# Kernel optimization log

Hardware: AMD Instinct MI355X
Metric: run time of the kernel (lower is better)

## Reference

```python
import jax, jax.numpy as jnp
import numpy as np

# Model hyperparameters (match init_kwargs)
T = 3          # reasoning hops
L = 3          # rule channels (parallel LSTMs)
E = 50000      # number of entities
N = 1000000    # number of KG triples
R = 200        # r_size = (n-1)//2
NREL = 2 * R + 1  # n = 401 (forward rels, inverse rels, identity)
H = 256        # emb_size
TAU = 10.0     # tau_1 softmax temperature
TOPK = 1000    # top-k state pruning for hops t>=1
B = 8          # batch size


def setup_inputs() -> dict:
    key = jax.random.key(0)
    ks = jax.random.split(key, 16)
    s = 0.05
    return {
        "input_x": jax.random.randint(ks[0], (B,), 0, E),
        "input_r": jax.random.randint(ks[1], (B,), 0, NREL),
        "e2triple": jax.random.randint(ks[2], (3, N), 0, E),
        "triple2e": jax.random.randint(ks[3], (2, N), 0, E),
        "r2triple": jax.random.randint(ks[4], (1, N), 0, R),
        "emb": jax.random.normal(ks[5], (NREL, H), jnp.float32) * s,
        "Wih_f": jax.random.normal(ks[6], (L, 4 * H, H), jnp.float32) * s,
        "Whh_f": jax.random.normal(ks[7], (L, 4 * H, H), jnp.float32) * s,
        "bih_f": jax.random.normal(ks[8], (L, 4 * H), jnp.float32) * s,
        "bhh_f": jax.random.normal(ks[9], (L, 4 * H), jnp.float32) * s,
        "Wih_b": jax.random.normal(ks[10], (L, 4 * H, H), jnp.float32) * s,
        "Whh_b": jax.random.normal(ks[11], (L, 4 * H, H), jnp.float32) * s,
        "bih_b": jax.random.normal(ks[12], (L, 4 * H), jnp.float32) * s,
        "bhh_b": jax.random.normal(ks[13], (L, 4 * H), jnp.float32) * s,
        "linW": jax.random.normal(ks[14], (NREL, 2 * H), jnp.float32) * s,
        "linb": jax.random.normal(ks[15], (NREL,), jnp.float32) * s,
    }


def _lstm_scan(x, Wih, Whh, bih, bhh):
    # x: [S, B, H]; PyTorch gate order i, f, g, o. Returns hidden seq [S, B, H].
    Bn = x.shape[1]
    Hh = Whh.shape[1]
    pre = x @ Wih.T + bih + bhh  # hoist input projection out of the scan

    def step(carry, xt):
        h, c = carry
        g = xt + h @ Whh.T
        i, f, gg, o = jnp.split(g, 4, axis=-1)
        c = jax.nn.sigmoid(f) * c + jax.nn.sigmoid(i) * jnp.tanh(gg)
        h = jax.nn.sigmoid(o) * jnp.tanh(c)
        return (h, c), h

    init = (jnp.zeros((Bn, Hh), x.dtype), jnp.zeros((Bn, Hh), x.dtype))
    _, hs = jax.lax.scan(step, init, pre)
    return hs


def reference(input_x, input_r, e2triple, triple2e, r2triple, emb,
              Wih_f, Whh_f, bih_f, bhh_f, Wih_b, Whh_b, bih_b, bhh_b,
              linW, linb):
    Bsz = input_x.shape[0]
    x0 = jax.nn.one_hot(input_x, E, dtype=emb.dtype)  # [B, E] one-hot query entity
    q = emb[input_r]                                   # [B, H] query relation emb
    # [T+1, B, H]: T copies of the query rel emb, last step is the special emb[-1]
    seq = jnp.concatenate([
        jnp.broadcast_to(q[None], (T, Bsz, H)),
        jnp.broadcast_to(emb[-1][None, None, :], (1, Bsz, H)),
    ], axis=0)

    outs = []
    for l in range(L):  # small fixed number of structurally distinct LSTMs
        hf = _lstm_scan(seq, Wih_f[l], Whh_f[l], bih_f[l], bhh_f[l])
        hb = _lstm_scan(seq[::-1], Wih_b[l], Whh_b[l], bih_b[l], bhh_b[l])[::-1]
        rnn = jnp.concatenate([hf, hb], axis=-1).transpose(1, 0, 2)  # [B, T+1, 2H]
        outs.append(rnn[:, :-1] @ linW.T + linb)                      # [B, T, n]
    w_all = jnp.stack(outs, axis=2)  # [B, T, L, n]

    heads = e2triple[0]   # [N] head entity per triple
    tails = triple2e[1]   # [N] tail entity per triple
    tails2 = e2triple[2]  # [N] tail entity per triple (inverse-direction gather)
    rels = r2triple[0]    # [N] relation per triple, in [0, R)

    def propagate(x, w):
        # x: [B, *, E] entity state, w: [B, L, n] relation weights
        s_i = w[:, :, -1:] * x                              # identity relation
        msg_f = x[:, :, heads] * w[:, :, rels]              # [B, L, N] fwd messages
        s_h = jnp.zeros((Bsz, L, E), x.dtype).at[:, :, tails].add(msg_f)
        msg_b = x[:, :, tails2] * w[:, :, rels + R]         # inverse relations
        s_t = jnp.zeros((Bsz, L, E), x.dtype).at[:, :, heads].add(msg_b)
        return s_i + s_h + s_t

    def prune_topk(x, k):
        # keep top-k entity scores per (batch, channel), zero the rest
        th = jax.lax.top_k(x, k)[0][..., -1:]
        return jnp.where(x >= th, x, jnp.zeros((), x.dtype))

    s = None
    for t in range(T):
        w = jax.nn.softmax(w_all[:, t] / TAU, axis=-1)      # [B, L, n]
        xin = x0[:, None, :] if t == 0 else prune_topk(s, TOPK)
        st = propagate(xin, w)
        s = st / jnp.maximum(st.sum(-1, keepdims=True), 1e-7)
    return s.sum(axis=1)  # [B, E]
```

## Files before the change

kernel.cpp:

```cpp
#include <hip/hip_runtime.h>
#include <math.h>

#define TT 3
#define LL 3
#define EE 50000
#define NN 1000000
#define RR 200
#define NRELC 401
#define HH 256
#define BB 8
#define KTOP 1000
#define SROW 24
#define NBUCK 782
#define BSH 6
#define CSRN (2 * NN)
#define STB 512
#define SEGS 50176

__device__ __forceinline__ float sigmoidf_(float x) {
    if (x >= 0.f) { return 1.f / (1.f + expf(-x)); }
    float z = expf(x); return z / (1.f + z);
}

__global__ __launch_bounds__(256) void pre_fused(
    const int* __restrict__ input_r, const float* __restrict__ emb,
    const float* __restrict__ Wih_f, const float* __restrict__ bih_f, const float* __restrict__ bhh_f,
    const float* __restrict__ Wih_b, const float* __restrict__ bih_b, const float* __restrict__ bhh_b,
    float* __restrict__ preq, float* __restrict__ pree,
    float* __restrict__ hstate, float* __restrict__ cstate, float* __restrict__ hbuf2,
    const int* __restrict__ heads, const int* __restrict__ tails,
    unsigned* __restrict__ bh, int do_hist)
{
    if (blockIdx.x >= 384) {
        if (!do_hist) return;
        __shared__ unsigned h[NBUCK];
        int tid = threadIdx.x;
        int bid = blockIdx.x - 384;
        for (int i = tid; i < NBUCK; i += 256) h[i] = 0u;
        __syncthreads();
        for (int i = bid * 256 + tid; i < NN; i += STB * 256) {
            atomicAdd(&h[tails[i] >> BSH], 1u);
            atomicAdd(&h[heads[i] >> BSH], 1u);
        }
        __syncthreads();
        for (int j = tid; j < NBUCK; j += 256)
            bh[(size_t)j * STB + bid] = h[j];
        return;
    }
    int wave = blockIdx.x * 4 + (threadIdx.x >> 6);
    int lane = threadIdx.x & 63;
    int ld = wave >> 8;
    int j  = wave & 255;
    int l = ld >> 1, dir = ld & 1;
    const float* Wih = (dir ? Wih_b : Wih_f) + (size_t)l * 4 * HH * HH;
    const float* bih = (dir ? bih_b : bih_f) + l * 4 * HH;
    const float* bhh = (dir ? bhh_b : bhh_f) + l * 4 * HH;

    float4 xf[9];
    for (int b = 0; b < 8; ++b) {
        int r = input_r[b];
        xf[b] = *(const float4*)(emb + (size_t)r * HH + lane * 4);
    }
    xf[8] = *(const float4*)(emb + (size_t)(NRELC - 1) * HH + lane * 4);

    float g4[4], ge4[4];
    for (int q = 0; q < 4; ++q) {
        int row = q * 256 + j;
        float4 w4 = *(const float4*)(Wih + (size_t)row * HH + lane * 4);
        float acc[9];
        #pragma unroll
        for (int c = 0; c < 9; ++c)
            acc[c] = w4.x * xf[c].x + w4.y * xf[c].y + w4.z * xf[c].z + w4.w * xf[c].w;
        #pragma unroll
        for (int off = 32; off > 0; off >>= 1)
            #pragma unroll
            for (int c = 0; c < 9; ++c) acc[c] += __shfl_xor(acc[c], off);
        float bsum = bih[row] + bhh[row];
        g4[q]  = (lane < 8 ? acc[lane] : 0.f) + bsum;
        ge4[q] = acc[8] + bsum;
        if (lane < 8) preq[((size_t)ld * 8 + lane) * 1024 + row] = g4[q];
        if (lane == 8) pree[(size_t)ld * 1024 + row] = ge4[q];
    }
    if (lane < 8) {
        float gi, gg, go;
        if (dir == 0) { gi = g4[0]; gg = g4[2]; go = g4[3]; }
        else          { gi = ge4[0]; gg = ge4[2]; go = ge4[3]; }
        float c = sigmoidf_(gi) * tanhf(gg);
        float h = sigmoidf_(go) * tanhf(c);
        int g = (ld * 8 + lane) * 256 + j;
        cstate[g] = c;
        hstate[g] = h;
        if (dir == 0) hbuf2[(((size_t)ld * 8 + lane) * 3 + 0) * HH + j] = h;
    }
}

__global__ __launch_bounds__(256) void rec_fused(
    const float* __restrict__ Whh_f, const float* __restrict__ Whh_b,
    const float* __restrict__ preq, const float* __restrict__ pree,
    const float* __restrict__ hprev, float* __restrict__ hnext,
    float* __restrict__ cstate, float* __restrict__ hbuf2, int step)
{
    int wave = blockIdx.x * 4 + (threadIdx.x >> 6);
    int lane = threadIdx.x & 63;
    int ld = wave >> 8, j = wave & 255;
    int l = ld >> 1, dir = ld & 1;
    const float* Whh = (dir ? Whh_b : Whh_f) + (size_t)l * 4 * HH * HH;
    bool use_e = (dir == 0) && (step == 3);

    float4 hf[8];
    for (int b = 0; b < 8; ++b)
        hf[b] = *(const float4*)(hprev + ((size_t)ld * 8 + b) * HH + lane * 4);

    float g4[4];
    for (int q = 0; q < 4; ++q) {
        int row = q * 256 + j;
        float4 w4 = *(const float4*)(Whh + (size_t)row * HH + lane * 4);
        float acc[8];
        #pragma unroll
        for (int b = 0; b < 8; ++b)
            acc[b] = w4.x * hf[b].x + w4.y * hf[b].y + w4.z * hf[b].z + w4.w * hf[b].w;
        #pragma unroll
        for (int off = 32; off > 0; off >>= 1)
            #pragma unroll
            for (int b = 0; b < 8; ++b) acc[b] += __shfl_xor(acc[b], off);
        if (lane < 8) {
            float pre = use_e ? pree[(size_t)ld * 1024 + row]
                              : preq[((size_t)ld * 8 + lane) * 1024 + row];
            g4[q] = acc[lane] + pre;
        }
    }
    if (lane < 8) {
        int g = (ld * 8 + lane) * 256 + j;
        float c = cstate[g];
        float iv = sigmoidf_(g4[0]), fv = sigmoidf_(g4[1]);
        float gg = tanhf(g4[2]),     ov = sigmoidf_(g4[3]);
        c = fv * c + iv * gg;
        float h = ov * tanhf(c);
        cstate[g] = c;
        hnext[g] = h;
        int t_out = dir ? (3 - step) : step;
        if (t_out <= 2) hbuf2[(((size_t)ld * 8 + lane) * 3 + t_out) * HH + j] = h;
    }
}

__global__ __launch_bounds__(256) void logits_dot(
    const float* __restrict__ hbuf2, const float* __restrict__ linW,
    const float* __restrict__ linb, float* __restrict__ wbuf)
{
    int wave = blockIdx.x * 4 + (threadIdx.x >> 6);
    if (wave >= 3 * 3 * NRELC) return;
    int lane = threadIdx.x & 63;
    int n = wave % NRELC;
    int tc = wave / NRELC;
    int t = tc / 3, chunk = tc % 3;
    const float4* wr = (const float4*)(linW + (size_t)n * 2 * HH + lane * 8);
    float4 w4a = wr[0], w4b = wr[1];
    float acc[8];
    #pragma unroll
    for (int i = 0; i < 8; ++i) {
        int combo = chunk * 8 + i;
        int b = combo / 3, l = combo % 3;
        int ldh = (lane < 32) ? (l * 2 + 0) : (l * 2 + 1);
        const float* hsrc = hbuf2 + (((size_t)ldh * 8 + b) * 3 + t) * HH + (lane & 31) * 8;
        float4 f0 = *(const float4*)hsrc;
        float4 f1 = *(const float4*)(hsrc + 4);
        acc[i] = w4a.x * f0.x + w4a.y * f0.y + w4a.z * f0.z + w4a.w * f0.w
               + w4b.x * f1.x + w4b.y * f1.y + w4b.z * f1.z + w4b.w * f1.w;
    }
    #pragma unroll
    for (int off = 32; off > 0; off >>= 1)
        #pragma unroll
        for (int i = 0; i < 8; ++i) acc[i] += __shfl_xor(acc[i], off);
    if (lane < 8) {
        int combo = chunk * 8 + lane;
        wbuf[((size_t)t * 24 + combo) * NRELC + n] = acc[lane] + linb[n];
    }
}

__global__ __launch_bounds__(256) void softmax_kernel(
    float* __restrict__ wbuf, float* __restrict__ wT0,
    int* __restrict__ maskT0, int* __restrict__ maskT1, int* __restrict__ maskT2,
    const int* __restrict__ input_x, unsigned* __restrict__ rowcnt)
{
    int tid = threadIdx.x;
    if (blockIdx.x >= 72) {
        if (maskT0 == nullptr) return;
        __shared__ int xs[8];
        if (tid < 8) xs[tid] = input_x[tid];
        if (blockIdx.x == 72 && tid < 24) rowcnt[tid] = 0u;
        __syncthreads();
        int e = (blockIdx.x - 72) * 256 + tid;
        if (e >= EE) return;
        int m = 0;
        #pragma unroll
        for (int b = 0; b < 8; ++b) if (e == xs[b]) m |= 1 << b;
        maskT0[e] = m;
        maskT1[e] = 0;
        maskT2[e] = 0;
        return;
    }
    int rowi = blockIdx.x;
    float* w = wbuf + (size_t)rowi * NRELC;
    __shared__ float red[256];
    float v0 = w[tid];
    float v1 = (tid + 256 < NRELC) ? w[tid + 256] : -1e30f;
    red[tid] = fmaxf(v0, v1); __syncthreads();
    for (int s2 = 128; s2 > 0; s2 >>= 1) {
        if (tid < s2) red[tid] = fmaxf(red[tid], red[tid + s2]);
        __syncthreads();
    }
    float m = red[0]; __syncthreads();
    float e0 = expf((v0 - m) * 0.1f);
    float e1 = (tid + 256 < NRELC) ? expf((v1 - m) * 0.1f) : 0.f;
    red[tid] = e0 + e1; __syncthreads();
    for (int s2 = 128; s2 > 0; s2 >>= 1) {
        if (tid < s2) red[tid] += red[tid + s2];
        __syncthreads();
    }
    float denom = red[0];
    float o0 = e0 / denom;
    w[tid] = o0;
    float o1 = 0.f;
    if (tid + 256 < NRELC) { o1 = e1 / denom; w[tid + 256] = o1; }
    if (wT0 != nullptr && rowi < 24) {
        if (tid < 2 * RR) wT0[(size_t)tid * SROW + rowi] = o0;
        if (tid + 256 < 2 * RR) wT0[(size_t)(tid + 256) * SROW + rowi] = o1;
    }
}

__global__ __launch_bounds__(256) void fill_seed(
    float* __restrict__ s, const int* __restrict__ input_x, const float* __restrict__ w0,
    unsigned* __restrict__ rowcnt)
{
    __shared__ int xs[8];
    __shared__ float wv[24];
    if (threadIdx.x < 8) xs[threadIdx.x] = input_x[threadIdx.x];
    if (threadIdx.x < 24) wv[threadIdx.x] = w0[(size_t)threadIdx.x * NRELC + (NRELC - 1)];
    if (blockIdx.x == 0 && threadIdx.x < 24) rowcnt[threadIdx.x] = 0u;
    __syncthreads();
    int i = blockIdx.x * 256 + threadIdx.x;
    if (i >= SROW * EE) return;
    int row = i % 24;
    int e = i / 24;
    s[i] = (e == xs[row / 3]) ? wv[row] : 0.f;
}

__global__ __launch_bounds__(256) void hop0_scan(
    const int* __restrict__ heads, const int* __restrict__ tails,
    const int* __restrict__ tails2, const int* __restrict__ rels,
    const int* __restrict__ input_x, const float* __restrict__ w0,
    float* __restrict__ s)
{
    __shared__ int xs[BB];
    if (threadIdx.x < BB) xs[threadIdx.x] = input_x[threadIdx.x];
    __syncthreads();
    int i = blockIdx.x * 256 + threadIdx.x;
    if (i >= NN) return;
    int h = heads[i], t2 = tails2[i];
    bool any = false;
    #pragma unroll
    for (int b = 0; b < BB; ++b) any = any || (h == xs[b]) || (t2 == xs[b]);
    if (!any) return;
    int tl = tails[i], rr = rels[i];
    for (int b = 0; b < BB; ++b) {
        if (h == xs[b])
            for (int l = 0; l < LL; ++l)
                atomicAdd(&s[(size_t)tl * SROW + b * 3 + l], w0[(b * 3 + l) * NRELC + rr]);
        if (t2 == xs[b])
            for (int l = 0; l < LL; ++l)
                atomicAdd(&s[(size_t)h * SROW + b * 3 + l], w0[(b * 3 + l) * NRELC + rr + RR]);
    }
}

__global__ __launch_bounds__(256) void rowsum_compact(
    const float* __restrict__ s, float* __restrict__ partial,
    unsigned* __restrict__ ckey, unsigned* __restrict__ rowcnt, int do_compact)
{
    __shared__ float acc[24];
    __shared__ unsigned lkey[24][168];
    __shared__ unsigned lcnt[24];
    __shared__ unsigned lbase[24];
    int tid = threadIdx.x;
    if (tid < 24) { acc[tid] = 0.f; lcnt[tid] = 0u; }
    __syncthreads();
    int gidx = blockIdx.x * 256 + tid;
    int row = gidx % 24;
    float a = 0.f;
    const int total = SROW * EE;
    for (int k = 0; k < 13; ++k) {
        long i = (long)gidx + (long)k * 98304;
        if (i < total) {
            float v = s[i];
            a += v;
            if (do_compact && __float_as_uint(v) != 0u) {
                unsigned slot = atomicAdd(&lcnt[row], 1u);
                slot = min(slot, 167u);
                lkey[row][slot] = __float_as_uint(v);
            }
        }
    }
    if (do_compact) {
        __syncthreads();
        if (tid < 24) {
            unsigned c = min(lcnt[tid], 168u);
            lcnt[tid] = c;
            lbase[tid] = min(atomicAdd(&rowcnt[tid], c), (unsigned)SEGS);
        }
        __syncthreads();
        int r = tid % 24;
        int nthr = (r < 16) ? 11 : 10;
        unsigned cnt = lcnt[r], base = lbase[r];
        if (base + cnt > (unsigned)SEGS) cnt = (unsigned)SEGS - base;
        for (unsigned j = (unsigned)(tid / 24); j < cnt; j += nthr)
            ckey[(size_t)r * SEGS + base + j] = lkey[r][j];
        __syncthreads();
    }
    atomicAdd(&acc[row], a);
    __syncthreads();
    if (tid < 24) partial[blockIdx.x * 24 + tid] = acc[tid];
}

__global__ __launch_bounds__(256) void rowsum_fin(
    const float* __restrict__ partial, float* __restrict__ sums,
    const float* __restrict__ w_t, float* __restrict__ wsc,
    float* __restrict__ wTg)
{
    int r = blockIdx.x;
    int tid = threadIdx.x;
    __shared__ float sa;
    if (tid == 0) {
        float a = 0.f;
        for (int j = 0; j < 384; ++j) a += partial[j * 24 + r];
        a = fmaxf(a, 1e-7f);
        sums[r] = a;
        sa = a;
    }
    __syncthreads();
    if (w_t != nullptr) {
        float a = sa;
        for (int i = tid; i < NRELC; i += 256) {
            float v = w_t[(size_t)r * NRELC + i] / a;
            wsc[(size_t)r * NRELC + i] = v;
            if (wTg != nullptr && i < 2 * RR) wTg[(size_t)i * SROW + r] = v;
        }
    }
}

__global__ __launch_bounds__(256) void rowsum_fin2(
    const float* __restrict__ partial2, float* __restrict__ sums,
    const float* __restrict__ w_t, float* __restrict__ wsc,
    float* __restrict__ wTg)
{
    int r = blockIdx.x;
    int tid = threadIdx.x;
    __shared__ float red[256];
    float a = 0.f;
    for (int g = tid; g < NBUCK; g += 256) a += partial2[(size_t)g * 24 + r];
    red[tid] = a; __syncthreads();
    for (int s2 = 128; s2 > 0; s2 >>= 1) {
        if (tid < s2) red[tid] += red[tid + s2];
        __syncthreads();
    }
    __shared__ float sa;
    if (tid == 0) { sa = fmaxf(red[0], 1e-7f); sums[r] = sa; }
    __syncthreads();
    if (w_t != nullptr) {
        float aa = sa;
        for (int i = tid; i < NRELC; i += 256) {
            float v = w_t[(size_t)r * NRELC + i] / aa;
            wsc[(size_t)r * NRELC + i] = v;
            if (wTg != nullptr && i < 2 * RR) wTg[(size_t)i * SROW + r] = v;
        }
    }
}

__global__ __launch_bounds__(512) void hop_epi(
    const unsigned* __restrict__ ckey, const unsigned* __restrict__ cent,
    unsigned* __restrict__ rowcnt, float* __restrict__ th,
    int* __restrict__ mask_next,
    const float* __restrict__ partial2, float* __restrict__ sums,
    const float* __restrict__ w_t, float* __restrict__ wsc,
    float* __restrict__ wTg)
{
    int tid = threadIdx.x;
    if (blockIdx.x >= 24) {
        int r = blockIdx.x - 24;
        __shared__ float red[256];
        __shared__ float sa;
        if (tid < 256) {
            float a = 0.f;
            for (int g = tid; g < NBUCK; g += 256) a += partial2[(size_t)g * 24 + r];
            red[tid] = a;
        }
        __syncthreads();
        for (int s2 = 128; s2 > 0; s2 >>= 1) {
            if (tid < s2) red[tid] += red[tid + s2];
            __syncthreads();
        }
        if (tid == 0) { sa = fmaxf(red[0], 1e-7f); sums[r] = sa; }
        __syncthreads();
        float aa = sa;
        for (int i = tid; i < NRELC; i += 512) {
            float v = w_t[(size_t)r * NRELC + i] / aa;
            wsc[(size_t)r * NRELC + i] = v;
            if (i < 2 * RR) wTg[(size_t)i * SROW + r] = v;
        }
        return;
    }
    int row = blockIdx.x;
    const unsigned* keys = ckey + (size_t)row * SEGS;
    int n = min((int)rowcnt[row], SEGS);
    __shared__ unsigned hist[256];
    __shared__ int red[256];
    __shared__ int sh_bin, sh_rem;
    unsigned prefix = 0;
    int remk = KTOP;
    int iters = (n + 511) / 512;
    int lane = tid & 63;
    for (int round = 0; round < 4; ++round) {
        if (tid < 256) hist[tid] = 0u;
        __syncthreads();
        int shift = 24 - 8 * round;
        for (int it = 0; it < iters; ++it) {
            int i = it * 512 + tid;
            bool valid = (i < n);
            unsigned key = valid ? keys[i] : 0u;
            valid = valid && (round == 0 || (key >> (shift + 8)) == prefix);
            unsigned bin = valid ? ((key >> shift) & 255u) : 0u;
            unsigned long long peers = __ballot(valid);
            #pragma unroll
            for (int bit = 0; bit < 8; ++bit) {
                unsigned long long bm = __ballot(valid && ((bin >> bit) & 1u));
                peers &= ((bin >> bit) & 1u) ? bm : ~bm;
            }
            if (valid) {
                unsigned long long lower = peers & ((1ull << lane) - 1ull);
                if (lower == 0ull)
                    atomicAdd(&hist[bin], (unsigned)__popcll(peers));
            }
        }
        __syncthreads();
        if (tid < 256) red[tid] = (int)hist[tid];
        __syncthreads();
        for (int off = 1; off < 256; off <<= 1) {
            int v = 0;
            if (tid < 256 && tid + off < 256) v = red[tid + off];
            __syncthreads();
            if (tid < 256) red[tid] += v;
            __syncthreads();
        }
        if (tid == 0) { sh_bin = 0; sh_rem = remk; }
        __syncthreads();
        if (tid < 256) {
            int cnt = (int)hist[tid];
            int above = (tid == 255) ? 0 : red[tid + 1];
            if (above < remk && above + cnt >= remk) { sh_bin = tid; sh_rem = remk - above; }
        }
        __syncthreads();
        prefix = (prefix << 8) | (unsigned)sh_bin;
        remk = sh_rem;
        __syncthreads();
    }
    if (tid == 0) th[row] = __uint_as_float(prefix);
    {
        const unsigned* ents = cent + (size_t)row * SEGS;
        int bit = 1 << (row / 3);
        for (int i = tid; i < n; i += 512) {
            if (keys[i] >= prefix) {
                unsigned e = ents[i];
                if (e < (unsigned)EE) atomicOr(&mask_next[e], bit);
            }
        }
        if (tid == 0) rowcnt[row] = 0u;
    }
}

__global__ __launch_bounds__(512) void topk_select(
    const unsigned* __restrict__ ckey, unsigned* __restrict__ rowcnt,
    float* __restrict__ th, int* __restrict__ mask)
{
    int row = blockIdx.x, tid = threadIdx.x;
    {
        int per = (EE + 23) / 24;
        int e0 = row * per, e1 = min(e0 + per, EE);
        for (int e = e0 + tid; e < e1; e += 512) mask[e] = 0;
    }
    const unsigned* keys = ckey + (size_t)row * SEGS;
    int n = min((int)rowcnt[row], SEGS);
    __shared__ unsigned hist[256];
    __shared__ int red[256];
    __shared__ int sh_bin, sh_rem;
    unsigned prefix = 0;
    int remk = KTOP;
    int iters = (n + 511) / 512;
    int lane = tid & 63;
    for (int round = 0; round < 4; ++round) {
        if (tid < 256) hist[tid] = 0u;
        __syncthreads();
        int shift = 24 - 8 * round;
        for (int it = 0; it < iters; ++it) {
            int i = it * 512 + tid;
            bool valid = (i < n);
            unsigned key = valid ? keys[i] : 0u;
            valid = valid && (round == 0 || (key >> (shift + 8)) == prefix);
            unsigned bin = valid ? ((key >> shift) & 255u) : 0u;
            unsigned long long peers = __ballot(valid);
            #pragma unroll
            for (int bit = 0; bit < 8; ++bit) {
                unsigned long long bm = __ballot(valid && ((bin >> bit) & 1u));
                peers &= ((bin >> bit) & 1u) ? bm : ~bm;
            }
            if (valid) {
                unsigned long long lower = peers & ((1ull << lane) - 1ull);
                if (lower == 0ull)
                    atomicAdd(&hist[bin], (unsigned)__popcll(peers));
            }
        }
        __syncthreads();
        if (tid < 256) red[tid] = (int)hist[tid];
        __syncthreads();
        for (int off = 1; off < 256; off <<= 1) {
            int v = 0;
            if (tid < 256 && tid + off < 256) v = red[tid + off];
            __syncthreads();
            if (tid < 256) red[tid] += v;
            __syncthreads();
        }
        if (tid == 0) { sh_bin = 0; sh_rem = remk; }
        __syncthreads();
        if (tid < 256) {
            int cnt = (int)hist[tid];
            int above = (tid == 255) ? 0 : red[tid + 1];
            if (above < remk && above + cnt >= remk) { sh_bin = tid; sh_rem = remk - above; }
        }
        __syncthreads();
        prefix = (prefix << 8) | (unsigned)sh_bin;
        remk = sh_rem;
        __syncthreads();
    }
    if (tid == 0) th[row] = __uint_as_float(prefix);
}

__global__ __launch_bounds__(256) void prune_flat(
    float* __restrict__ s, const float* __restrict__ th,
    const float* __restrict__ wsc, float* __restrict__ x, int* __restrict__ mask,
    unsigned* __restrict__ rowcnt, int write_s)
{
    __shared__ float ths[24], w4s[24];
    if (threadIdx.x < 24) {
        ths[threadIdx.x] = th[threadIdx.x];
        w4s[threadIdx.x] = wsc[threadIdx.x * NRELC + (NRELC - 1)];
    }
    if (blockIdx.x == 0 && threadIdx.x < 24) rowcnt[threadIdx.x] = 0u;
    __syncthreads();
    int i = blockIdx.x * 256 + threadIdx.x;
    if (i >= SROW * EE) return;
    int row = i % 24;
    int e = i / 24;
    float v = s[i];
    float xv = (v >= ths[row]) ? v : 0.f;
    x[i] = xv;
    if (write_s) s[i] = w4s[row] * xv;
    if (xv > 0.f) atomicOr(&mask[e], 1 << (row / 3));
}

__global__ __launch_bounds__(256) void hop_scan(
    const int* __restrict__ heads, const int* __restrict__ tails,
    const int* __restrict__ tails2, const int* __restrict__ rels,
    const int* __restrict__ mask, const float* __restrict__ x,
    const float* __restrict__ wsc, float* __restrict__ s)
{
    int gid = blockIdx.x * 256 + threadIdx.x;
    int i = gid >> 3;
    if (i >= NN) return;
    int b = gid & 7;
    int h = heads[i], t2 = tails2[i];
    int mh = mask[h], mt = mask[t2];
    bool ah = (mh >> b) & 1;
    bool at = (mt >> b) & 1;
    if (!(ah || at)) return;
    int tl = tails[i], rr = rels[i];
    int row = b * 3;
    if (ah) {
        float v0 = x[(size_t)h * SROW + row];
        float v1 = x[(size_t)h * SROW + row + 1];
        float v2 = x[(size_t)h * SROW + row + 2];
        if (v0 != 0.f) atomicAdd(&s[(size_t)tl * SROW + row],     v0 * wsc[(row)     * NRELC + rr]);
        if (v1 != 0.f) atomicAdd(&s[(size_t)tl * SROW + row + 1], v1 * wsc[(row + 1) * NRELC + rr]);
        if (v2 != 0.f) atomicAdd(&s[(size_t)tl * SROW + row + 2], v2 * wsc[(row + 2) * NRELC + rr]);
    }
    if (at) {
        float v0 = x[(size_t)t2 * SROW + row];
        float v1 = x[(size_t)t2 * SROW + row + 1];
        float v2 = x[(size_t)t2 * SROW + row + 2];
        if (v0 != 0.f) atomicAdd(&s[(size_t)h * SROW + row],     v0 * wsc[(row)     * NRELC + rr + RR]);
        if (v1 != 0.f) atomicAdd(&s[(size_t)h * SROW + row + 1], v1 * wsc[(row + 1) * NRELC + rr + RR]);
        if (v2 != 0.f) atomicAdd(&s[(size_t)h * SROW + row + 2], v2 * wsc[(row + 2) * NRELC + rr + RR]);
    }
}

__global__ __launch_bounds__(512) void csr_scanb(
    unsigned* __restrict__ bh, unsigned* __restrict__ gcnt)
{
    __shared__ unsigned sc[STB];
    int bk = blockIdx.x, tid = threadIdx.x;
    unsigned v = bh[(size_t)bk * STB + tid];
    sc[tid] = v; __syncthreads();
    #pragma unroll
    for (int o = 1; o < STB; o <<= 1) {
        unsigned u = (tid >= o) ? sc[tid - o] : 0u;
        __syncthreads();
        sc[tid] += u;
        __syncthreads();
    }
    bh[(size_t)bk * STB + tid] = sc[tid] - v;
    if (tid == STB - 1) gcnt[bk] = sc[tid];
}

__global__ __launch_bounds__(1024) void csr_scan2(
    const unsigned* __restrict__ gcnt, unsigned* __restrict__ gOff)
{
    __shared__ unsigned sc[1024];
    int tid = threadIdx.x;
    unsigned v = (tid < NBUCK) ? gcnt[tid] : 0u;
    sc[tid] = v; __syncthreads();
    #pragma unroll
    for (int o = 1; o < 1024; o <<= 1) {
        unsigned u = (tid >= o) ? sc[tid - o] : 0u;
        __syncthreads();
        sc[tid] += u;
        __syncthreads();
    }
    if (tid < NBUCK) gOff[tid] = sc[tid] - v;
    if (tid == NBUCK - 1) gOff[NBUCK] = sc[tid];
}

__global__ __launch_bounds__(256) void csr_stage2(
    const int* __restrict__ heads, const int* __restrict__ tails,
    const int* __restrict__ tails2, const int* __restrict__ rels,
    const unsigned* __restrict__ gOff, const unsigned* __restrict__ bh,
    unsigned* __restrict__ staging)
{
    __shared__ unsigned base[NBUCK];
    __shared__ unsigned cur[NBUCK];
    int tid = threadIdx.x;
    for (int j = tid; j < NBUCK; j += 256) {
        base[j] = gOff[j] + bh[(size_t)j * STB + blockIdx.x];
        cur[j] = 0u;
    }
    __syncthreads();
    for (int i = blockIdx.x * 256 + tid; i < NN; i += STB * 256) {
        unsigned rl = (unsigned)rels[i];
        int h = heads[i], d1 = tails[i], t2 = tails2[i];
        unsigned p1 = base[d1 >> BSH] + atomicAdd(&cur[d1 >> BSH], 1u);
        if (p1 < (unsigned)CSRN)
            staging[p1] = ((unsigned)(d1 & 63) << 26) | ((unsigned)h << 9) | rl;
        unsigned p2 = base[h >> BSH] + atomicAdd(&cur[h >> BSH], 1u);
        if (p2 < (unsigned)CSRN)
            staging[p2] = ((unsigned)(h & 63) << 26) | ((unsigned)t2 << 9) | (rl + RR);
    }
}

__global__ __launch_bounds__(256) void hop_bucket(
    const unsigned* __restrict__ gOff, const unsigned* __restrict__ staging,
    const int* __restrict__ mask, const float* __restrict__ sprev,
    const float* __restrict__ th, const int* __restrict__ input_x,
    const float* __restrict__ wT, const float* __restrict__ wsc,
    float* __restrict__ snext, float* __restrict__ partial2,
    unsigned* __restrict__ ckey, unsigned* __restrict__ cent,
    unsigned* __restrict__ rowcnt, int do_compact, int is_t0)
{
    __shared__ float sl[64][24];
    __shared__ float w4s[24];
    __shared__ float ths[24];
    __shared__ int   xs8[8];
    __shared__ float acc24[24];
    __shared__ unsigned lcnt[24];
    __shared__ unsigned lbase[24];
    __shared__ unsigned lkey[24][64];
    __shared__ unsigned lent[24][64];
    int bk = blockIdx.x, tid = threadIdx.x;
    for (int i = tid; i < 64 * 24; i += 256) ((float*)sl)[i] = 0.f;
    if (tid < 24) {
        w4s[tid] = wsc[tid * NRELC + (NRELC - 1)];
        ths[tid] = is_t0 ? 0.f : th[tid];
        acc24[tid] = 0.f;
        lcnt[tid] = 0u;
    }
    if (tid < 8) xs8[tid] = is_t0 ? input_x[tid] : 0;
    __syncthreads();
    unsigned j0 = gOff[bk], j1 = gOff[bk + 1];
    for (unsigned j = j0 + tid; j < j1; j += 256) {
        unsigned p = staging[j];
        int src = (int)((p >> 9) & 0xFFFFu);
        int m = mask[src];
        if (!m) continue;
        int dl = (int)(p >> 26);
        int rel = (int)(p & 511u);
        const float* wr = wT + (size_t)rel * SROW;
        if (is_t0) {
            while (m) {
                int b = __ffs(m) - 1; m &= m - 1;
                int r = b * 3;
                atomicAdd(&sl[dl][r],     wr[r]);
                atomicAdd(&sl[dl][r + 1], wr[r + 1]);
                atomicAdd(&sl[dl][r + 2], wr[r + 2]);
            }
        } else {
            const float* xsrow = sprev + (size_t)src * SROW;
            while (m) {
                int b = __ffs(m) - 1; m &= m - 1;
                int r = b * 3;
                float x0 = xsrow[r];     x0 = (x0 >= ths[r])     ? x0 : 0.f;
                float x1 = xsrow[r + 1]; x1 = (x1 >= ths[r + 1]) ? x1 : 0.f;
                float x2 = xsrow[r + 2]; x2 = (x2 >= ths[r + 2]) ? x2 : 0.f;
                atomicAdd(&sl[dl][r],     x0 * wr[r]);
                atomicAdd(&sl[dl][r + 1], x1 * wr[r + 1]);
                atomicAdd(&sl[dl][r + 2], x2 * wr[r + 2]);
            }
        }
    }
    __syncthreads();
    int e0 = bk * 64;
    for (int idx = tid; idx < 64 * 24; idx += 256) {
        int el = idx / 24, row = idx % 24;
        int e = e0 + el;
        if (e >= EE) continue;
        float xv;
        if (is_t0) {
            xv = (e == xs8[row / 3]) ? 1.f : 0.f;
        } else {
            float u = sprev[(size_t)e * SROW + row];
            xv = (u >= ths[row]) ? u : 0.f;
        }
        float v = sl[el][row] + w4s[row] * xv;
        snext[(size_t)e * SROW + row] = v;
        atomicAdd(&acc24[row], v);
        if (do_compact && __float_as_uint(v) != 0u) {
            unsigned slot = atomicAdd(&lcnt[row], 1u);
            slot = min(slot, 63u);
            lkey[row][slot] = __float_as_uint(v);
            lent[row][slot] = (unsigned)e;
        }
    }
    __syncthreads();
    if (tid < 24) partial2[(size_t)bk * 24 + tid] = acc24[tid];
    if (do_compact) {
        if (tid < 24) {
            unsigned c = min(lcnt[tid], 64u);
            lcnt[tid] = c;
            lbase[tid] = min(atomicAdd(&rowcnt[tid], c), (unsigned)SEGS);
        }
        __syncthreads();
        int r = tid % 24;
        int nthr = (r < 16) ? 11 : 10;
        unsigned cnt = lcnt[r], base = lbase[r];
        if (base + cnt > (unsigned)SEGS) cnt = (unsigned)SEGS - base;
        for (unsigned j = (unsigned)(tid / 24); j < cnt; j += nthr) {
            ckey[(size_t)r * SEGS + base + j] = lkey[r][j];
            cent[(size_t)r * SEGS + base + j] = lent[r][j];
        }
    }
}

__global__ void final_kernel(const float* __restrict__ s, const float* __restrict__ sums,
                             float* __restrict__ out) {
    __shared__ float ss[24];
    if (threadIdx.x < 24) ss[threadIdx.x] = sums[threadIdx.x];
    __syncthreads();
    int e = blockIdx.x * 256 + threadIdx.x;
    if (e >= EE) return;
    const float* se = s + (size_t)e * SROW;
    #pragma unroll
    for (int b = 0; b < 8; ++b)
        out[(size_t)b * EE + e] = se[b * 3] / ss[b * 3]
                                + se[b * 3 + 1] / ss[b * 3 + 1]
                                + se[b * 3 + 2] / ss[b * 3 + 2];
}

extern "C" void kernel_launch(void* const* d_in, const int* in_sizes, int n_in,
                              void* d_out, int out_size, void* d_ws, size_t ws_size,
                              hipStream_t stream)
{
    const int*   input_x  = (const int*)d_in[0];
    const int*   input_r  = (const int*)d_in[1];
    const int*   e2triple = (const int*)d_in[2];
    const int*   triple2e = (const int*)d_in[3];
    const int*   r2triple = (const int*)d_in[4];
    const float* emb      = (const float*)d_in[5];
    const float* Wih_f    = (const float*)d_in[6];
    const float* Whh_f    = (const float*)d_in[7];
    const float* bih_f    = (const float*)d_in[8];
    const float* bhh_f    = (const float*)d_in[9];
    const float* Wih_b    = (const float*)d_in[10];
    const float* Whh_b    = (const float*)d_in[11];
    const float* bih_b    = (const float*)d_in[12];
    const float* bhh_b    = (const float*)d_in[13];
    const float* linW     = (const float*)d_in[14];
    const float* linb     = (const float*)d_in[15];

    const int* heads  = e2triple;
    const int* tails2 = e2triple + 2 * (size_t)NN;
    const int* tails  = triple2e + (size_t)NN;
    const int* rels   = r2triple;

    float* ws      = (float*)d_ws;
    float* hbuf    = ws;
    float* wbuf    = hbuf + 36864;
    float* sstA    = wbuf + 28872;
    float* sstB    = sstA + 1200000;
    float* sums    = sstB + 1200000;
    float* th      = sums + 24;
    int*   maskT0  = (int*)(th + 24);
    int*   maskT1  = maskT0 + EE;
    int*   maskT2  = maskT1 + EE;
    float* partial = (float*)(maskT2 + EE);
    unsigned* rowcnt  = (unsigned*)(partial + 9216);
    float* partial2   = (float*)(rowcnt + 32);
    unsigned* ckey    = (unsigned*)(partial2 + NBUCK * 24);
    unsigned* cent    = ckey + 24 * (size_t)SEGS;
    unsigned* bh      = cent + 24 * (size_t)SEGS;
    unsigned* gcnt    = bh + (size_t)NBUCK * STB;
    unsigned* gOff    = gcnt + 784;
    unsigned* staging = gOff + 800;
    float*    wT      = (float*)(staging + CSRN);
    float*    wT0     = wT + 9600;
    const size_t NEED = (size_t)((wT0 + 9600) - ws) * 4;
    const bool use_csr = (ws_size >= NEED);
    float* wsc     = hbuf;
    float* preq    = sstA;
    float* pree    = preq + 49152;
    float* hstateA = pree + 6144;
    float* hstateB = hstateA + 12288;
    float* cstate  = hstateB + 12288;

    float* out = (float*)d_out;
    const int EBLK  = (EE + 255) / 256;
    const int SBLK  = (SROW * EE + 255) / 256;
    const int NBLK  = (NN + 255) / 256;
    const int N8BLK = (NN * 8) / 256;

    pre_fused<<<896, 256, 0, stream>>>(input_r, emb, Wih_f, bih_f, bhh_f,
                                       Wih_b, bih_b, bhh_b, preq, pree,
                                       hstateA, cstate, hbuf,
                                       heads, tails, bh, use_csr ? 1 : 0);
    rec_fused<<<384, 256, 0, stream>>>(Whh_f, Whh_b, preq, pree, hstateA, hstateB,
                                       cstate, hbuf, 1);
    rec_fused<<<384, 256, 0, stream>>>(Whh_f, Whh_b, preq, pree, hstateB, hstateA,
                                       cstate, hbuf, 2);
    rec_fused<<<384, 256, 0, stream>>>(Whh_f, Whh_b, preq, pree, hstateA, hstateB,
                                       cstate, hbuf, 3);
    logits_dot<<<903, 256, 0, stream>>>(hbuf, linW, linb, wbuf);

    if (use_csr) {
        softmax_kernel<<<72 + EBLK, 256, 0, stream>>>(wbuf, wT0, maskT0, maskT1, maskT2,
                                                      input_x, rowcnt);
        csr_scanb<<<NBUCK, 512, 0, stream>>>(bh, gcnt);
        csr_scan2<<<1, 1024, 0, stream>>>(gcnt, gOff);
        csr_stage2<<<STB, 256, 0, stream>>>(heads, tails, tails2, rels, gOff, bh, staging);
        hop_bucket<<<NBUCK, 256, 0, stream>>>(gOff, staging, maskT0, nullptr, nullptr,
                                              input_x, wT0, wbuf, sstA, partial2,
                                              ckey, cent, rowcnt, 1, 1);
        hop_epi<<<48, 512, 0, stream>>>(ckey, cent, rowcnt, th, maskT1,
                                        partial2, sums, wbuf + 1 * 24 * NRELC, wsc, wT);
        hop_bucket<<<NBUCK, 256, 0, stream>>>(gOff, staging, maskT1, sstA, th,
                                              input_x, wT, wsc, sstB, partial2,
                                              ckey, cent, rowcnt, 1, 0);
        hop_epi<<<48, 512, 0, stream>>>(ckey, cent, rowcnt, th, maskT2,
                                        partial2, sums, wbuf + 2 * 24 * NRELC, wsc, wT);
        hop_bucket<<<NBUCK, 256, 0, stream>>>(gOff, staging, maskT2, sstB, th,
                                              input_x, wT, wsc, sstA, partial2,
                                              ckey, cent, rowcnt, 0, 0);
        rowsum_fin2<<<24, 256, 0, stream>>>(partial2, sums, nullptr, nullptr, nullptr);
        final_kernel<<<EBLK, 256, 0, stream>>>(sstA, sums, out);
    } else {
        softmax_kernel<<<72, 256, 0, stream>>>(wbuf, nullptr, nullptr, nullptr, nullptr,
                                               input_x, rowcnt);
        float* xst = sstA;
        float* sst = sstB;
        int* mask = maskT0;
        fill_seed<<<SBLK, 256, 0, stream>>>(sst, input_x, wbuf, rowcnt);
        hop0_scan<<<NBLK, 256, 0, stream>>>(heads, tails, tails2, rels, input_x, wbuf, sst);
        rowsum_compact<<<384, 256, 0, stream>>>(sst, partial, ckey, rowcnt, 1);
        rowsum_fin<<<24, 256, 0, stream>>>(partial, sums, wbuf + 1 * 24 * NRELC, wsc, nullptr);
        for (int t = 1; t < TT; ++t) {
            topk_select<<<24, 512, 0, stream>>>(ckey, rowcnt, th, mask);
            prune_flat<<<SBLK, 256, 0, stream>>>(sst, th, wsc, xst, mask, rowcnt, 1);
            hop_scan<<<N8BLK, 256, 0, stream>>>(heads, tails, tails2, rels, mask, xst, wsc, sst);
            rowsum_compact<<<384, 256, 0, stream>>>(sst, partial, ckey, rowcnt,
                                                    (t + 1 < TT) ? 1 : 0);
            const float* w_next = (t + 1 < TT) ? (wbuf + (size_t)(t + 1) * 24 * NRELC) : nullptr;
            rowsum_fin<<<24, 256, 0, stream>>>(partial, sums, w_next, wsc, nullptr);
        }
        final_kernel<<<EBLK, 256, 0, stream>>>(sst, sums, out);
    }
}
```

Before: 289.4 us.

## Fuse CSR build stages into logits and softmax kernels, merge final rowsum

```diff
diff --git a/kernel.cpp b/kernel.cpp
--- a/kernel.cpp
+++ b/kernel.cpp
@@ -16,6 +16,7 @@
 #define CSRN (2 * NN)
 #define STB 512
 #define SEGS 50176
+#define EBLK ((EE + 255) / 256)
 
 __device__ __forceinline__ float sigmoidf_(float x) {
     if (x >= 0.f) { return 1.f / (1.f + expf(-x)); }
@@ -145,11 +146,35 @@
 
 __global__ __launch_bounds__(256) void logits_dot(
     const float* __restrict__ hbuf2, const float* __restrict__ linW,
-    const float* __restrict__ linb, float* __restrict__ wbuf)
-{
-    int wave = blockIdx.x * 4 + (threadIdx.x >> 6);
+    const float* __restrict__ linb, float* __restrict__ wbuf,
+    unsigned* __restrict__ bh, unsigned* __restrict__ gcnt)
+{
+    int tid = threadIdx.x;
+    if (blockIdx.x >= 903) {
+        if (gcnt == nullptr) return;
+        int bk = blockIdx.x - 903;
+        unsigned a = bh[(size_t)bk * STB + 2 * tid];
+        unsigned b = bh[(size_t)bk * STB + 2 * tid + 1];
+        unsigned s = a + b;
+        __shared__ unsigned sc[256];
+        sc[tid] = s; __syncthreads();
+        #pragma unroll
+        for (int off = 1; off < 256; off <<= 1) {
+            unsigned u = (tid >= off) ? sc[tid - off] : 0u;
+            __syncthreads();
+            sc[tid] += u;
+            __syncthreads();
+        }
+        unsigned incl = sc[tid];
+        unsigned ex = incl - s;
+        bh[(size_t)bk * STB + 2 * tid]     = ex;
+        bh[(size_t)bk * STB + 2 * tid + 1] = ex + a;
+        if (tid == 255) gcnt[bk] = incl;
+        return;
+    }
+    int wave = blockIdx.x * 4 + (tid >> 6);
     if (wave >= 3 * 3 * NRELC) return;
-    int lane = threadIdx.x & 63;
+    int lane = tid & 63;
     int n = wave % NRELC;
     int tc = wave / NRELC;
     int t = tc / 3, chunk = tc % 3;
@@ -180,9 +205,62 @@
 __global__ __launch_bounds__(256) void softmax_kernel(
     float* __restrict__ wbuf, float* __restrict__ wT0,
     int* __restrict__ maskT0, int* __restrict__ maskT1, int* __restrict__ maskT2,
-    const int* __restrict__ input_x, unsigned* __restrict__ rowcnt)
+    const int* __restrict__ input_x, unsigned* __restrict__ rowcnt,
+    const int* __restrict__ heads, const int* __restrict__ tails,
+    const int* __restrict__ tails2, const int* __restrict__ rels,
+    const unsigned* __restrict__ bh, const unsigned* __restrict__ gcnt,
+    unsigned* __restrict__ gOff, unsigned* __restrict__ staging)
 {
     int tid = threadIdx.x;
+    if (blockIdx.x >= 72 + EBLK) {
+        int bid = blockIdx.x - (72 + EBLK);
+        __shared__ unsigned sv[1024];
+        __shared__ unsigned base[NBUCK];
+        __shared__ unsigned cur[NBUCK];
+        unsigned orig[4];
+        #pragma unroll
+        for (int k = 0; k < 4; ++k) {
+            int j = tid + k * 256;
+            unsigned v = (j < NBUCK) ? gcnt[j] : 0u;
+            orig[k] = v; sv[j] = v;
+        }
+        __syncthreads();
+        for (int off = 1; off < 1024; off <<= 1) {
+            unsigned t4[4];
+            #pragma unroll
+            for (int k = 0; k < 4; ++k) {
+                int j = tid + k * 256;
+                t4[k] = (j >= off) ? sv[j - off] : 0u;
+            }
+            __syncthreads();
+            #pragma unroll
+            for (int k = 0; k < 4; ++k) sv[tid + k * 256] += t4[k];
+            __syncthreads();
+        }
+        #pragma unroll
+        for (int k = 0; k < 4; ++k) {
+            int j = tid + k * 256;
+            if (j < NBUCK) {
+                unsigned ex = sv[j] - orig[k];
+                base[j] = ex + bh[(size_t)j * STB + bid];
+                cur[j] = 0u;
+                if (bid == 0) gOff[j] = ex;
+            }
+        }
+        if (bid == 0 && tid == 0) gOff[NBUCK] = sv[1023];
+        __syncthreads();
+        for (int i = bid * 256 + tid; i < NN; i += STB * 256) {
+            unsigned rl = (unsigned)rels[i];
+            int h = heads[i], d1 = tails[i], t2 = tails2[i];
+            unsigned p1 = base[d1 >> BSH] + atomicAdd(&cur[d1 >> BSH], 1u);
+            if (p1 < (unsigned)CSRN)
+                staging[p1] = ((unsigned)(d1 & 63) << 26) | ((unsigned)h << 9) | rl;
+            unsigned p2 = base[h >> BSH] + atomicAdd(&cur[h >> BSH], 1u);
+            if (p2 < (unsigned)CSRN)
+                staging[p2] = ((unsigned)(h & 63) << 26) | ((unsigned)t2 << 9) | (rl + RR);
+        }
+        return;
+    }
     if (blockIdx.x >= 72) {
         if (maskT0 == nullptr) return;
         __shared__ int xs[8];
@@ -340,34 +418,6 @@
         float a = sa;
         for (int i = tid; i < NRELC; i += 256) {
             float v = w_t[(size_t)r * NRELC + i] / a;
-            wsc[(size_t)r * NRELC + i] = v;
-            if (wTg != nullptr && i < 2 * RR) wTg[(size_t)i * SROW + r] = v;
-        }
-    }
-}
-
-__global__ __launch_bounds__(256) void rowsum_fin2(
-    const float* __restrict__ partial2, float* __restrict__ sums,
-    const float* __restrict__ w_t, float* __restrict__ wsc,
-    float* __restrict__ wTg)
-{
-    int r = blockIdx.x;
-    int tid = threadIdx.x;
-    __shared__ float red[256];
-    float a = 0.f;
-    for (int g = tid; g < NBUCK; g += 256) a += partial2[(size_t)g * 24 + r];
-    red[tid] = a; __syncthreads();
-    for (int s2 = 128; s2 > 0; s2 >>= 1) {
-        if (tid < s2) red[tid] += red[tid + s2];
-        __syncthreads();
-    }
-    __shared__ float sa;
-    if (tid == 0) { sa = fmaxf(red[0], 1e-7f); sums[r] = sa; }
-    __syncthreads();
-    if (w_t != nullptr) {
-        float aa = sa;
-        for (int i = tid; i < NRELC; i += 256) {
-            float v = w_t[(size_t)r * NRELC + i] / aa;
             wsc[(size_t)r * NRELC + i] = v;
             if (wTg != nullptr && i < 2 * RR) wTg[(size_t)i * SROW + r] = v;
         }
@@ -596,68 +646,6 @@
         if (v0 != 0.f) atomicAdd(&s[(size_t)h * SROW + row],     v0 * wsc[(row)     * NRELC + rr + RR]);
         if (v1 != 0.f) atomicAdd(&s[(size_t)h * SROW + row + 1], v1 * wsc[(row + 1) * NRELC + rr + RR]);
         if (v2 != 0.f) atomicAdd(&s[(size_t)h * SROW + row + 2], v2 * wsc[(row + 2) * NRELC + rr + RR]);
-    }
-}
-
-__global__ __launch_bounds__(512) void csr_scanb(
-    unsigned* __restrict__ bh, unsigned* __restrict__ gcnt)
-{
-    __shared__ unsigned sc[STB];
-    int bk = blockIdx.x, tid = threadIdx.x;
-    unsigned v = bh[(size_t)bk * STB + tid];
-    sc[tid] = v; __syncthreads();
-    #pragma unroll
-    for (int o = 1; o < STB; o <<= 1) {
-        unsigned u = (tid >= o) ? sc[tid - o] : 0u;
-        __syncthreads();
-        sc[tid] += u;
-        __syncthreads();
-    }
-    bh[(size_t)bk * STB + tid] = sc[tid] - v;
-    if (tid == STB - 1) gcnt[bk] = sc[tid];
-}
-
-__global__ __launch_bounds__(1024) void csr_scan2(
-    const unsigned* __restrict__ gcnt, unsigned* __restrict__ gOff)
-{
-    __shared__ unsigned sc[1024];
-    int tid = threadIdx.x;
-    unsigned v = (tid < NBUCK) ? gcnt[tid] : 0u;
-    sc[tid] = v; __syncthreads();
-    #pragma unroll
-    for (int o = 1; o < 1024; o <<= 1) {
-        unsigned u = (tid >= o) ? sc[tid - o] : 0u;
-        __syncthreads();
-        sc[tid] += u;
-        __syncthreads();
-    }
-    if (tid < NBUCK) gOff[tid] = sc[tid] - v;
-    if (tid == NBUCK - 1) gOff[NBUCK] = sc[tid];
-}
-
-__global__ __launch_bounds__(256) void csr_stage2(
-    const int* __restrict__ heads, const int* __restrict__ tails,
-    const int* __restrict__ tails2, const int* __restrict__ rels,
-    const unsigned* __restrict__ gOff, const unsigned* __restrict__ bh,
-    unsigned* __restrict__ staging)
-{
-    __shared__ unsigned base[NBUCK];
-    __shared__ unsigned cur[NBUCK];
-    int tid = threadIdx.x;
-    for (int j = tid; j < NBUCK; j += 256) {
-        base[j] = gOff[j] + bh[(size_t)j * STB + blockIdx.x];
-        cur[j] = 0u;
-    }
-    __syncthreads();
-    for (int i = blockIdx.x * 256 + tid; i < NN; i += STB * 256) {
-        unsigned rl = (unsigned)rels[i];
-        int h = heads[i], d1 = tails[i], t2 = tails2[i];
-        unsigned p1 = base[d1 >> BSH] + atomicAdd(&cur[d1 >> BSH], 1u);
-        if (p1 < (unsigned)CSRN)
-            staging[p1] = ((unsigned)(d1 & 63) << 26) | ((unsigned)h << 9) | rl;
-        unsigned p2 = base[h >> BSH] + atomicAdd(&cur[h >> BSH], 1u);
-        if (p2 < (unsigned)CSRN)
-            staging[p2] = ((unsigned)(h & 63) << 26) | ((unsigned)t2 << 9) | (rl + RR);
     }
 }
 
@@ -778,6 +766,32 @@
                                 + se[b * 3 + 2] / ss[b * 3 + 2];
 }
 
+__global__ __launch_bounds__(256) void final_fused(
+    const float* __restrict__ s, const float* __restrict__ partial2,
+    float* __restrict__ out)
+{
+    __shared__ float ss[24];
+    int tid = threadIdx.x;
+    if (tid < 192) {
+        int r = tid >> 3, sub = tid & 7;
+        float a = 0.f;
+        for (int g = sub; g < NBUCK; g += 8) a += partial2[(size_t)g * 24 + r];
+        a += __shfl_xor(a, 1);
+        a += __shfl_xor(a, 2);
+        a += __shfl_xor(a, 4);
+        if (sub == 0) ss[r] = fmaxf(a, 1e-7f);
+    }
+    __syncthreads();
+    int e = blockIdx.x * 256 + tid;
+    if (e >= EE) return;
+    const float* se = s + (size_t)e * SROW;
+    #pragma unroll
+    for (int b = 0; b < 8; ++b)
+        out[(size_t)b * EE + e] = se[b * 3] / ss[b * 3]
+                                + se[b * 3 + 1] / ss[b * 3 + 1]
+                                + se[b * 3 + 2] / ss[b * 3 + 2];
+}
+
 extern "C" void kernel_launch(void* const* d_in, const int* in_sizes, int n_in,
                               void* d_out, int out_size, void* d_ws, size_t ws_size,
                               hipStream_t stream)
@@ -835,7 +849,6 @@
     float* cstate  = hstateB + 12288;
 
     float* out = (float*)d_out;
-    const int EBLK  = (EE + 255) / 256;
     const int SBLK  = (SROW * EE + 255) / 256;
     const int NBLK  = (NN + 255) / 256;
     const int N8BLK = (NN * 8) / 256;
@@ -850,14 +863,12 @@
                                        cstate, hbuf, 2);
     rec_fused<<<384, 256, 0, stream>>>(Whh_f, Whh_b, preq, pree, hstateA, hstateB,
                                        cstate, hbuf, 3);
-    logits_dot<<<903, 256, 0, stream>>>(hbuf, linW, linb, wbuf);
 
     if (use_csr) {
-        softmax_kernel<<<72 + EBLK, 256, 0, stream>>>(wbuf, wT0, maskT0, maskT1, maskT2,
-                                                      input_x, rowcnt);
-        csr_scanb<<<NBUCK, 512, 0, stream>>>(bh, gcnt);
-        csr_scan2<<<1, 1024, 0, stream>>>(gcnt, gOff);
-        csr_stage2<<<STB, 256, 0, stream>>>(heads, tails, tails2, rels, gOff, bh, staging);
+        logits_dot<<<903 + NBUCK, 256, 0, stream>>>(hbuf, linW, linb, wbuf, bh, gcnt);
+        softmax_kernel<<<72 + EBLK + STB, 256, 0, stream>>>(
+            wbuf, wT0, maskT0, maskT1, maskT2, input_x, rowcnt,
+            heads, tails, tails2, rels, bh, gcnt, gOff, staging);
         hop_bucket<<<NBUCK, 256, 0, stream>>>(gOff, staging, maskT0, nullptr, nullptr,
                                               input_x, wT0, wbuf, sstA, partial2,
                                               ckey, cent, rowcnt, 1, 1);
@@ -871,11 +882,12 @@
         hop_bucket<<<NBUCK, 256, 0, stream>>>(gOff, staging, maskT2, sstB, th,
                                               input_x, wT, wsc, sstA, partial2,
                                               ckey, cent, rowcnt, 0, 0);
-        rowsum_fin2<<<24, 256, 0, stream>>>(partial2, sums, nullptr, nullptr, nullptr);
-        final_kernel<<<EBLK, 256, 0, stream>>>(sstA, sums, out);
+        final_fused<<<EBLK, 256, 0, stream>>>(sstA, partial2, out);
     } else {
+        logits_dot<<<903, 256, 0, stream>>>(hbuf, linW, linb, wbuf, nullptr, nullptr);
         softmax_kernel<<<72, 256, 0, stream>>>(wbuf, nullptr, nullptr, nullptr, nullptr,
-                                               input_x, rowcnt);
+                                               input_x, rowcnt, heads, tails, tails2,
+                                               rels, bh, gcnt, gOff, staging);
         float* xst = sstA;
         float* sst = sstB;
         int* mask = maskT0;
```

Result: slower. 317.4 us (+9.7%).
